# Kernel tuning notes

Hardware: AMD Instinct MI355X
Metric: run time of the kernel (lower is better)

Reference implementation:

```python
import jax, jax.numpy as jnp
import numpy as np

N = 50000      # total nodes
E = 800000     # directed edges
G = 512        # graphs in batch
F_IN = 64      # node feature dim
H = 128        # hidden dim
L = 3          # gnn layers
OUT = 12       # tox21 tasks
EPS = 1e-5


def layer_norm(h, gamma, beta):
    mu = jnp.mean(h, axis=-1, keepdims=True)
    var = jnp.mean(jnp.square(h - mu), axis=-1, keepdims=True)
    return (h - mu) * jax.lax.rsqrt(var + EPS) * gamma + beta


def setup_inputs() -> dict:
    key = jax.random.key(0)
    ks = jax.random.split(key, 20)
    x = jax.random.normal(ks[0], (N, F_IN), jnp.float32)
    edge_index = jax.random.randint(ks[1], (2, E), 0, N, dtype=jnp.int64)
    batch_ids = jnp.sort(jax.random.randint(ks[2], (N,), 0, G, dtype=jnp.int64))
    s_in = 1.0 / np.sqrt(F_IN)
    s_h = 1.0 / np.sqrt(H)
    return {
        "x": x,
        "edge_index": edge_index,
        "batch_ids": batch_ids,
        "W_embed": jax.random.normal(ks[3], (F_IN, H), jnp.float32) * s_in,
        "b_embed": jnp.zeros((H,), jnp.float32),
        "g_embed": jnp.ones((H,), jnp.float32),
        "be_embed": jnp.zeros((H,), jnp.float32),
        "W_conv": jax.random.normal(ks[4], (L, H, H), jnp.float32) * s_h,
        "b_conv": jnp.zeros((L, H), jnp.float32),
        "g_ln": jnp.ones((L, H), jnp.float32),
        "b_ln": jnp.zeros((L, H), jnp.float32),
        "W_r1": jax.random.normal(ks[5], (H, H // 2), jnp.float32) * s_h,
        "b_r1": jnp.zeros((H // 2,), jnp.float32),
        "W_r2": jax.random.normal(ks[6], (H // 2, OUT), jnp.float32) * (1.0 / np.sqrt(H // 2)),
        "b_r2": jnp.zeros((OUT,), jnp.float32),
    }


def reference(x, edge_index, batch_ids, W_embed, b_embed, g_embed, be_embed,
              W_conv, b_conv, g_ln, b_ln, W_r1, b_r1, W_r2, b_r2):
    n = x.shape[0]
    # node embedding: Linear -> LayerNorm -> ReLU (dropout = eval identity)
    h = jax.nn.relu(layer_norm(x @ W_embed + b_embed, g_embed, be_embed))

    # GCN normalization with self-loops (PyG GCNConv semantics)
    loop = jnp.arange(n, dtype=edge_index.dtype)
    src = jnp.concatenate([edge_index[0], loop])  # message sources
    dst = jnp.concatenate([edge_index[1], loop])  # message targets
    deg = jax.ops.segment_sum(jnp.ones_like(dst, dtype=h.dtype), dst, num_segments=N)
    dinv = jnp.where(deg > 0, jax.lax.rsqrt(deg), 0.0)
    norm = dinv[src] * dinv[dst]  # [E+N]

    for i in range(L):
        h_prev = h
        m = h @ W_conv[i]                                        # [N,H] linear first
        msg = m[src] * norm[:, None]                             # gather + scale
        agg = jax.ops.segment_sum(msg, dst, num_segments=N)      # scatter-add
        agg = agg + b_conv[i]                                    # bias after aggregation
        h = jax.nn.relu(layer_norm(agg, g_ln[i], b_ln[i])) + h_prev  # norm+relu+residual

    # global mean pooling per graph
    counts = jax.ops.segment_sum(jnp.ones((n,), h.dtype), batch_ids, num_segments=G)
    pooled = jax.ops.segment_sum(h, batch_ids, num_segments=G) / jnp.maximum(counts, 1.0)[:, None]

    # readout MLP
    r = jax.nn.relu(pooled @ W_r1 + b_r1)
    return r @ W_r2 + b_r2
```

## Files before the change

kernel.cpp:

```cpp
#include <hip/hip_runtime.h>

#define HDIM 128
#define FIN 64
#define EPS 1e-5f
#define ECH 2048
#define PITCH 64

typedef unsigned int uint;
typedef unsigned short ushort;
typedef __attribute__((ext_vector_type(8))) short bf16x8;
typedef __attribute__((ext_vector_type(4))) float f32x4;

__device__ __forceinline__ ushort f2bf(float f) {
    uint u = __float_as_uint(f);
    return (ushort)((u + 0x7fffu + ((u >> 16) & 1u)) >> 16);
}
__device__ __forceinline__ float bflo(uint u) { return __uint_as_float(u << 16); }
__device__ __forceinline__ float bfhi(uint u) { return __uint_as_float(u & 0xffff0000u); }

#define PART_OF(d) (((d) >> 4) & 7)

__global__ __launch_bounds__(256) void embed_fused(
    const float* __restrict__ x, const float* __restrict__ W,
    const float* __restrict__ b, const float* __restrict__ g,
    const float* __restrict__ be, ushort* __restrict__ hbf, int nrows,
    const int* __restrict__ src, const int* __restrict__ dst,
    int* __restrict__ fcnt, ushort* __restrict__ ell, int e,
    const float* __restrict__ Wc, ushort* __restrict__ Wt)
{
    int t = threadIdx.x;
    int gtid = blockIdx.x * 256 + t;
    if (gtid < 3 * HDIM * HDIM) {
        int l = gtid >> 14, rem = gtid & 16383;
        int k = rem >> 7, nn = rem & 127;
        Wt[(l << 14) + nn * HDIM + k] = f2bf(Wc[gtid]);
    }
    {
        int gpart = blockIdx.x & 7;
        int base2 = ((blockIdx.x >> 3) * ECH) >> 1;
        const int2* dst2 = (const int2*)dst;
        const int2* src2 = (const int2*)src;
#pragma unroll
        for (int i = 0; i < ECH / 2 / 256; i++) {
            int idx2 = base2 + t + i * 256;
            if (idx2 * 2 < e) {
                int2 dd = dst2[idx2];
                int2 ss = src2[idx2];
                if (PART_OF(dd.x) == gpart) {
                    int slot = atomicAdd(&fcnt[dd.x], 1);
                    if (slot < PITCH) ell[((size_t)dd.x << 6) + slot] = (ushort)ss.x;
                }
                if (idx2 * 2 + 1 < e && PART_OF(dd.y) == gpart) {
                    int slot = atomicAdd(&fcnt[dd.y], 1);
                    if (slot < PITCH) ell[((size_t)dd.y << 6) + slot] = (ushort)ss.y;
                }
            }
        }
    }

    int row0 = blockIdx.x * 32;
    if (row0 >= nrows) return;

    __shared__ ushort Ws[FIN * HDIM];
    __shared__ ushort xs[32 * FIN];
    {
        const float4* W4 = (const float4*)W;
        ushort4* Ws4 = (ushort4*)Ws;
#pragma unroll
        for (int i = 0; i < (FIN * HDIM / 4) / 256; i++) {
            float4 v = W4[t + i * 256];
            ushort4 o = { f2bf(v.x), f2bf(v.y), f2bf(v.z), f2bf(v.w) };
            Ws4[t + i * 256] = o;
        }
    }
    int nr = nrows - row0; if (nr > 32) nr = 32;
    {
        const float4* x4 = (const float4*)(x + (size_t)row0 * FIN);
        ushort4* xs4 = (ushort4*)xs;
        for (int i = t; i < nr * (FIN / 4); i += 256) {
            float4 v = x4[i];
            ushort4 o = { f2bf(v.x), f2bf(v.y), f2bf(v.z), f2bf(v.w) };
            xs4[i] = o;
        }
    }
    __syncthreads();

    int c = (t & 31) * 4;
    int r0 = (t >> 5) * 4;
    float acc[4][4];
    float4 bv = *(const float4*)(b + c);
#pragma unroll
    for (int i = 0; i < 4; i++) { acc[i][0] = bv.x; acc[i][1] = bv.y; acc[i][2] = bv.z; acc[i][3] = bv.w; }
#pragma unroll 8
    for (int k = 0; k < FIN; k++) {
        uint2 wu = *(const uint2*)(Ws + k * HDIM + c);
        float w0 = bflo(wu.x), w1 = bfhi(wu.x), w2 = bflo(wu.y), w3 = bfhi(wu.y);
#pragma unroll
        for (int i = 0; i < 4; i++) {
            float xv = __uint_as_float((uint)xs[(r0 + i) * FIN + k] << 16);
            acc[i][0] += xv * w0; acc[i][1] += xv * w1;
            acc[i][2] += xv * w2; acc[i][3] += xv * w3;
        }
    }
    float4 gv = *(const float4*)(g + c);
    float4 bev = *(const float4*)(be + c);
#pragma unroll
    for (int i = 0; i < 4; i++) {
        float s1 = acc[i][0] + acc[i][1] + acc[i][2] + acc[i][3];
        float s2 = acc[i][0]*acc[i][0] + acc[i][1]*acc[i][1] + acc[i][2]*acc[i][2] + acc[i][3]*acc[i][3];
#pragma unroll
        for (int m = 16; m; m >>= 1) { s1 += __shfl_xor(s1, m); s2 += __shfl_xor(s2, m); }
        float mu = s1 * (1.0f / HDIM);
        float var = s2 * (1.0f / HDIM) - mu * mu;
        float rstd = rsqrtf(var + EPS);
        int row = row0 + r0 + i;
        if (row < nrows) {
            float ox = fmaxf((acc[i][0] - mu) * rstd * gv.x + bev.x, 0.f);
            float oy = fmaxf((acc[i][1] - mu) * rstd * gv.y + bev.y, 0.f);
            float oz = fmaxf((acc[i][2] - mu) * rstd * gv.z + bev.z, 0.f);
            float ow = fmaxf((acc[i][3] - mu) * rstd * gv.w + bev.w, 0.f);
            uint2 hb;
            hb.x = ((uint)f2bf(oy) << 16) | f2bf(ox);
            hb.y = ((uint)f2bf(ow) << 16) | f2bf(oz);
            *(uint2*)(hbf + (size_t)row * HDIM + c) = hb;
        }
    }
}

__global__ __launch_bounds__(256) void gemm_mfma_kernel(
    const ushort* __restrict__ hbf, const ushort* __restrict__ Wt,
    const int* __restrict__ fcnt, ushort* __restrict__ mbf, int nrows)
{
    __shared__ ushort ws[HDIM * HDIM];
    int t = threadIdx.x;
    int wid = t >> 6, lane = t & 63;
    int row0 = blockIdx.x * 64;

#pragma unroll
    for (int it = 0; it < 8; it++) {
        int chunk = t * 8 + it;
        int r = chunk >> 4;
        int offb = (chunk & 15) * 16;
        uint4 d = *(const uint4*)(Wt + (size_t)r * HDIM + (offb >> 1));
        *(uint4*)((char*)ws + r * 256 + (offb ^ ((r & 7) << 4))) = d;
    }

    int arow = row0 + wid * 16 + (lane & 15);
    int arcl = (arow < nrows) ? arow : (nrows - 1);
    int kgrp = lane >> 4;
    const ushort* aptr = hbf + (size_t)arcl * HDIM + kgrp * 8;
    bf16x8 af[4];
#pragma unroll
    for (int ks = 0; ks < 4; ks++)
        af[ks] = *(const bf16x8*)(aptr + ks * 32);

    __syncthreads();

    f32x4 acc[8];
#pragma unroll
    for (int nt = 0; nt < 8; nt++) acc[nt] = (f32x4){0.f, 0.f, 0.f, 0.f};

    int kgb = kgrp * 16;
#pragma unroll
    for (int ks = 0; ks < 4; ks++) {
        int kb = ks * 64 + kgb;
#pragma unroll
        for (int nt = 0; nt < 8; nt++) {
            int nrow = nt * 16 + (lane & 15);
            bf16x8 bfrag = *(const bf16x8*)((const char*)ws + nrow * 256 + (kb ^ ((nrow & 7) << 4)));
            acc[nt] = __builtin_amdgcn_mfma_f32_16x16x32_bf16(af[ks], bfrag, acc[nt], 0, 0, 0);
        }
    }

    int rbase = row0 + wid * 16 + ((lane >> 4) << 2);
#pragma unroll
    for (int q = 0; q < 4; q++) {
        int grow = rbase + q;
        if (grow < nrows) {
            float dv = rsqrtf((float)(fcnt[grow] + 1));
            ushort* orow = mbf + (size_t)grow * HDIM + (lane & 15);
#pragma unroll
            for (int nt = 0; nt < 8; nt++)
                orow[nt * 16] = f2bf(acc[nt][q] * dv);
        }
    }
}

__global__ __launch_bounds__(256) void agg_kernel(
    const ushort* __restrict__ mbf, const ushort* __restrict__ ell, const int* __restrict__ fcnt,
    const float* __restrict__ bc,
    const float* __restrict__ gl, const float* __restrict__ bl,
    const ushort* __restrict__ hbf_in, ushort* __restrict__ hbf_out, int n)
{
    int wave = threadIdx.x >> 6, lane = threadIdx.x & 63;
    int v = blockIdx.x * 4 + wave;
    if (v >= n) return;
    const uint* m1 = (const uint*)mbf;
    uint hp = ((const uint*)hbf_in)[(size_t)v * 64 + lane];
    uint aa = m1[(size_t)v * 64 + lane];
    float ax = bflo(aa), ay = bfhi(aa);
    int deg = fcnt[v];
    const ushort* row = ell + ((size_t)v << 6);
    for (int base = 0; base < deg; base += 64) {
        int idx = base + lane;
        int my = (idx < deg) ? (int)row[idx] : 0;
        int cc = deg - base; if (cc > 64) cc = 64;
        int i = 0;
        for (; i + 4 <= cc; i += 4) {
            int u0 = __shfl(my, i);
            int u1 = __shfl(my, i + 1);
            int u2 = __shfl(my, i + 2);
            int u3 = __shfl(my, i + 3);
            uint w0 = m1[(size_t)u0 * 64 + lane];
            uint w1 = m1[(size_t)u1 * 64 + lane];
            uint w2 = m1[(size_t)u2 * 64 + lane];
            uint w3 = m1[(size_t)u3 * 64 + lane];
            ax += bflo(w0); ay += bfhi(w0);
            ax += bflo(w1); ay += bfhi(w1);
            ax += bflo(w2); ay += bfhi(w2);
            ax += bflo(w3); ay += bfhi(w3);
        }
        for (; i < cc; ++i) {
            int u0 = __shfl(my, i);
            uint w0 = m1[(size_t)u0 * 64 + lane];
            ax += bflo(w0); ay += bfhi(w0);
        }
    }
    float dvv = rsqrtf((float)(deg + 1));
    float2 bcv = ((const float2*)bc)[lane];
    float vx = ax * dvv + bcv.x;
    float vy = ay * dvv + bcv.y;
    float s1v = vx + vy, s2v = vx * vx + vy * vy;
#pragma unroll
    for (int m = 32; m; m >>= 1) { s1v += __shfl_xor(s1v, m); s2v += __shfl_xor(s2v, m); }
    float mu = s1v * (1.f / 128.f);
    float var = s2v * (1.f / 128.f) - mu * mu;
    float rstd = rsqrtf(var + EPS);
    float2 gv = ((const float2*)gl)[lane];
    float2 blv = ((const float2*)bl)[lane];
    float ox = fmaxf((vx - mu) * rstd * gv.x + blv.x, 0.f) + bflo(hp);
    float oy = fmaxf((vy - mu) * rstd * gv.y + blv.y, 0.f) + bfhi(hp);
    ((uint*)hbf_out)[(size_t)v * 64 + lane] = ((uint)f2bf(oy) << 16) | f2bf(ox);
}

__global__ __launch_bounds__(256) void pool_readout(
    const ushort* __restrict__ hbf, const int* __restrict__ batch,
    const float* __restrict__ W1, const float* __restrict__ b1,
    const float* __restrict__ W2, const float* __restrict__ b2,
    float* __restrict__ out, int n, int G)
{
    int g = blockIdx.x, t = threadIdx.x;
    int lo = 0, hi = n;
    while (lo < hi) { int mid = (lo + hi) >> 1; if (batch[mid] < g) lo = mid + 1; else hi = mid; }
    int lo2 = lo, hi2 = n;
    while (lo2 < hi2) { int mid = (lo2 + hi2) >> 1; if (batch[mid] < g + 1) lo2 = mid + 1; else hi2 = mid; }
    int cp = t & 63, portion = t >> 6;
    float accx = 0.f, accy = 0.f;
    const uint* h1 = (const uint*)hbf;
    for (int nd = lo + portion; nd < lo2; nd += 4) {
        uint u = h1[(size_t)nd * 64 + cp];
        accx += bflo(u); accy += bfhi(u);
    }
    float cntf = (float)(lo2 - lo); if (cntf < 1.f) cntf = 1.f;
    __shared__ float psx[256], psy[256];
    __shared__ float ps[HDIM];
    __shared__ float rs[64];
    psx[t] = accx; psy[t] = accy;
    __syncthreads();
    if (t < 64) {
        float px = psx[t] + psx[t + 64] + psx[t + 128] + psx[t + 192];
        float py = psy[t] + psy[t + 64] + psy[t + 128] + psy[t + 192];
        ps[2 * t]     = px / cntf;
        ps[2 * t + 1] = py / cntf;
    }
    __syncthreads();
    if (t < 64) {
        float a = b1[t];
#pragma unroll 4
        for (int k = 0; k < HDIM; k++) a += ps[k] * W1[k * 64 + t];
        rs[t] = fmaxf(a, 0.f);
    }
    __syncthreads();
    if (t < 12) {
        float a = b2[t];
#pragma unroll
        for (int k = 0; k < 64; k++) a += rs[k] * W2[k * 12 + t];
        out[(size_t)g * 12 + t] = a;
    }
}

extern "C" void kernel_launch(void* const* d_in, const int* in_sizes, int n_in,
                              void* d_out, int out_size, void* d_ws, size_t ws_size,
                              hipStream_t stream) {
    const float* x       = (const float*)d_in[0];
    const int*   ei      = (const int*)d_in[1];
    const int*   batch   = (const int*)d_in[2];
    const float* W_embed = (const float*)d_in[3];
    const float* b_embed = (const float*)d_in[4];
    const float* g_embed = (const float*)d_in[5];
    const float* be_emb  = (const float*)d_in[6];
    const float* W_conv  = (const float*)d_in[7];
    const float* b_conv  = (const float*)d_in[8];
    const float* g_ln    = (const float*)d_in[9];
    const float* b_ln    = (const float*)d_in[10];
    const float* W_r1    = (const float*)d_in[11];
    const float* b_r1    = (const float*)d_in[12];
    const float* W_r2    = (const float*)d_in[13];
    const float* b_r2    = (const float*)d_in[14];
    float* out = (float*)d_out;

    int N = in_sizes[2];
    int E = in_sizes[1] / 2;
    int G = out_size / 12;
    int npad = ((N + 255) / 256) * 256;

    char* w = (char*)d_ws;
    ushort* hbf0 = (ushort*)w;  w += (size_t)N * HDIM * 2;
    ushort* hbf1 = (ushort*)w;  w += (size_t)N * HDIM * 2;
    ushort* mbf  = (ushort*)w;  w += (size_t)N * HDIM * 2;
    ushort* Wt   = (ushort*)w;  w += (size_t)3 * HDIM * HDIM * 2;
    int* fcnt    = (int*)w;     w += (size_t)npad * 4;
    ushort* ell  = (ushort*)w;  w += (size_t)npad * PITCH * 2;

    int nchunks = (E + ECH - 1) / ECH;
    int gridEC = nchunks * 8;
    int gemmBlocks = (N + 63) / 64;

    hipMemsetAsync(fcnt, 0, (size_t)npad * 4, stream);

    embed_fused<<<gridEC, 256, 0, stream>>>(
        x, W_embed, b_embed, g_embed, be_emb, hbf0, N,
        ei, ei + E, fcnt, ell, E, W_conv, Wt);

    const ushort* hin = hbf0;
    ushort* hout = hbf1;
    for (int l = 0; l < 3; l++) {
        gemm_mfma_kernel<<<gemmBlocks, 256, 0, stream>>>(
            hin, Wt + (size_t)l * HDIM * HDIM, fcnt, mbf, N);
        agg_kernel<<<(N + 3) / 4, 256, 0, stream>>>(
            mbf, ell, fcnt, b_conv + l * HDIM, g_ln + l * HDIM, b_ln + l * HDIM,
            hin, hout, N);
        ushort* tmp = (ushort*)hin; hin = hout; hout = tmp;
    }
    pool_readout<<<G, 256, 0, stream>>>(hin, batch, W_r1, b_r1, W_r2, b_r2, out, N, G);
}
```

Measured before the change: 228.4 us.

## Fuse aggregation of layer l with the GEMM of layer l+1

Result: slower. 236.0 us (+3.3%).

```diff
diff --git a/kernel.cpp b/kernel.cpp
--- a/kernel.cpp
+++ b/kernel.cpp
@@ -182,6 +182,93 @@
 #pragma unroll
             for (int nt = 0; nt < 8; nt++)
                 orow[nt * 16] = f2bf(acc[nt][q] * dv);
+        }
+    }
+}
+
+__global__ __launch_bounds__(1024) void agg_gemm_kernel(
+    const ushort* __restrict__ mbf_in, const ushort* __restrict__ ell, const int* __restrict__ fcnt,
+    const float* __restrict__ bc,
+    const float* __restrict__ gl, const float* __restrict__ bl,
+    const ushort* __restrict__ hbf_in, ushort* __restrict__ hbf_out,
+    const ushort* __restrict__ Wt_next, ushort* __restrict__ mbf_out, int n)
+{
+    __shared__ ushort hs[16 * HDIM];
+    int wave = threadIdx.x >> 6, lane = threadIdx.x & 63;
+    int v = blockIdx.x * 16 + wave;
+    if (v < n) {
+        const uint* m1 = (const uint*)mbf_in;
+        uint hp = ((const uint*)hbf_in)[(size_t)v * 64 + lane];
+        uint aa = m1[(size_t)v * 64 + lane];
+        float ax = bflo(aa), ay = bfhi(aa);
+        int deg = fcnt[v];
+        const ushort* row = ell + ((size_t)v << 6);
+        for (int base = 0; base < deg; base += 64) {
+            int idx = base + lane;
+            int my = (idx < deg) ? (int)row[idx] : 0;
+            int cc = deg - base; if (cc > 64) cc = 64;
+            int i = 0;
+            for (; i + 4 <= cc; i += 4) {
+                int u0 = __shfl(my, i);
+                int u1 = __shfl(my, i + 1);
+                int u2 = __shfl(my, i + 2);
+                int u3 = __shfl(my, i + 3);
+                uint w0 = m1[(size_t)u0 * 64 + lane];
+                uint w1 = m1[(size_t)u1 * 64 + lane];
+                uint w2 = m1[(size_t)u2 * 64 + lane];
+                uint w3 = m1[(size_t)u3 * 64 + lane];
+                ax += bflo(w0); ay += bfhi(w0);
+                ax += bflo(w1); ay += bfhi(w1);
+                ax += bflo(w2); ay += bfhi(w2);
+                ax += bflo(w3); ay += bfhi(w3);
+            }
+            for (; i < cc; ++i) {
+                int u0 = __shfl(my, i);
+                uint w0 = m1[(size_t)u0 * 64 + lane];
+                ax += bflo(w0); ay += bfhi(w0);
+            }
+        }
+        float dvv = rsqrtf((float)(deg + 1));
+        float2 bcv = ((const float2*)bc)[lane];
+        float vx = ax * dvv + bcv.x;
+        float vy = ay * dvv + bcv.y;
+        float s1v = vx + vy, s2v = vx * vx + vy * vy;
+#pragma unroll
+        for (int m = 32; m; m >>= 1) { s1v += __shfl_xor(s1v, m); s2v += __shfl_xor(s2v, m); }
+        float mu = s1v * (1.f / 128.f);
+        float var = s2v * (1.f / 128.f) - mu * mu;
+        float rstd = rsqrtf(var + EPS);
+        float2 gv = ((const float2*)gl)[lane];
+        float2 blv = ((const float2*)bl)[lane];
+        float ox = fmaxf((vx - mu) * rstd * gv.x + blv.x, 0.f) + bflo(hp);
+        float oy = fmaxf((vy - mu) * rstd * gv.y + blv.y, 0.f) + bfhi(hp);
+        uint packed = ((uint)f2bf(oy) << 16) | f2bf(ox);
+        ((uint*)hbf_out)[(size_t)v * 64 + lane] = packed;
+        *(uint*)((char*)hs + wave * 256 + ((lane * 4) ^ ((wave & 7) << 4))) = packed;
+    }
+    __syncthreads();
+
+    if (wave < 8) {
+        int row0 = blockIdx.x * 16;
+        int arow = lane & 15;
+        int kg = lane >> 4;
+        f32x4 acc = (f32x4){0.f, 0.f, 0.f, 0.f};
+        const ushort* bp = Wt_next + (size_t)(wave * 16 + (lane & 15)) * HDIM + kg * 8;
+#pragma unroll
+        for (int ks = 0; ks < 4; ks++) {
+            int kb = ks * 64 + kg * 16;
+            bf16x8 af = *(const bf16x8*)((const char*)hs + arow * 256 + (kb ^ ((arow & 7) << 4)));
+            bf16x8 bf = *(const bf16x8*)(bp + ks * 32);
+            acc = __builtin_amdgcn_mfma_f32_16x16x32_bf16(af, bf, acc, 0, 0, 0);
+        }
+        int rb = (lane >> 4) << 2;
+#pragma unroll
+        for (int q = 0; q < 4; q++) {
+            int grow = row0 + rb + q;
+            if (grow < n) {
+                float dv = rsqrtf((float)(fcnt[grow] + 1));
+                mbf_out[(size_t)grow * HDIM + wave * 16 + (lane & 15)] = f2bf(acc[q] * dv);
+            }
         }
     }
 }
@@ -317,7 +404,8 @@
     char* w = (char*)d_ws;
     ushort* hbf0 = (ushort*)w;  w += (size_t)N * HDIM * 2;
     ushort* hbf1 = (ushort*)w;  w += (size_t)N * HDIM * 2;
-    ushort* mbf  = (ushort*)w;  w += (size_t)N * HDIM * 2;
+    ushort* mbf0 = (ushort*)w;  w += (size_t)N * HDIM * 2;
+    ushort* mbf1 = (ushort*)w;  w += (size_t)N * HDIM * 2;
     ushort* Wt   = (ushort*)w;  w += (size_t)3 * HDIM * HDIM * 2;
     int* fcnt    = (int*)w;     w += (size_t)npad * 4;
     ushort* ell  = (ushort*)w;  w += (size_t)npad * PITCH * 2;
@@ -325,6 +413,7 @@
     int nchunks = (E + ECH - 1) / ECH;
     int gridEC = nchunks * 8;
     int gemmBlocks = (N + 63) / 64;
+    int fusedBlocks = (N + 15) / 16;
 
     hipMemsetAsync(fcnt, 0, (size_t)npad * 4, stream);
 
@@ -332,15 +421,16 @@
         x, W_embed, b_embed, g_embed, be_emb, hbf0, N,
         ei, ei + E, fcnt, ell, E, W_conv, Wt);
 
-    const ushort* hin = hbf0;
-    ushort* hout = hbf1;
-    for (int l = 0; l < 3; l++) {
-        gemm_mfma_kernel<<<gemmBlocks, 256, 0, stream>>>(
-            hin, Wt + (size_t)l * HDIM * HDIM, fcnt, mbf, N);
-        agg_kernel<<<(N + 3) / 4, 256, 0, stream>>>(
-            mbf, ell, fcnt, b_conv + l * HDIM, g_ln + l * HDIM, b_ln + l * HDIM,
-            hin, hout, N);
-        ushort* tmp = (ushort*)hin; hin = hout; hout = tmp;
-    }
-    pool_readout<<<G, 256, 0, stream>>>(hin, batch, W_r1, b_r1, W_r2, b_r2, out, N, G);
-}
+    gemm_mfma_kernel<<<gemmBlocks, 256, 0, stream>>>(hbf0, Wt, fcnt, mbf0, N);
+    agg_gemm_kernel<<<fusedBlocks, 1024, 0, stream>>>(
+        mbf0, ell, fcnt, b_conv, g_ln, b_ln,
+        hbf0, hbf1, Wt + (size_t)1 * HDIM * HDIM, mbf1, N);
+    agg_gemm_kernel<<<fusedBlocks, 1024, 0, stream>>>(
+        mbf1, ell, fcnt, b_conv + HDIM, g_ln + HDIM, b_ln + HDIM,
+        hbf1, hbf0, Wt + (size_t)2 * HDIM * HDIM, mbf0, N);
+    agg_kernel<<<(N + 3) / 4, 256, 0, stream>>>(
+        mbf0, ell, fcnt, b_conv + 2 * HDIM, g_ln + 2 * HDIM, b_ln + 2 * HDIM,
+        hbf0, hbf1, N);
+
+    pool_readout<<<G, 256, 0, stream>>>(hbf1, batch, W_r1, b_r1, W_r2, b_r2, out, N, G);
+}
```
